# Performance work log

Measured on AMD Instinct MI355X. Metric: run time of the kernel, lower is better.

The kernel has to match this reference:

```python
import jax, jax.numpy as jnp
import numpy as np

N_NODES = 100000
N_EDGES = 1200000
D = 64
EPS = 1e-7
BETA = 1.0


def setup_inputs() -> dict:
    key = jax.random.key(0)
    k1, k2, k3, k4, k5 = jax.random.split(key, 5)
    node_feats = jax.random.normal(k1, (N_NODES, D), dtype=jnp.float32)
    edge_feats = jax.random.normal(k2, (N_EDGES, D), dtype=jnp.float32)
    W = jax.random.normal(k3, (D, D), dtype=jnp.float32) * (1.0 / np.sqrt(D))
    b = jnp.zeros((D,), dtype=jnp.float32)
    scale = jnp.ones((1,), dtype=jnp.float32)
    src = jax.random.randint(k4, (N_EDGES,), 0, N_NODES, dtype=jnp.int32)
    dst = jnp.sort(jax.random.randint(k5, (N_EDGES,), 0, N_NODES, dtype=jnp.int32))
    return {"node_feats": node_feats, "edge_feats": edge_feats, "W": W, "b": b,
            "scale": scale, "src": src, "dst": dst}


def reference(node_feats, edge_feats, W, b, scale, src, dst):
    # u_add_e: message = h[src] + edge_feats, then relu + eps  -> [E, D]
    m = jax.nn.relu(node_feats[src] + edge_feats) + EPS
    z = m * BETA
    # edge_softmax: per-destination, per-channel softmax over incoming edges
    mx = jax.ops.segment_max(z, dst, num_segments=N_NODES)      # [N, D]
    mx = jnp.where(jnp.isfinite(mx), mx, 0.0)                   # zero-degree guard
    e = jnp.exp(z - mx[dst])
    denom = jax.ops.segment_sum(e, dst, num_segments=N_NODES)   # [N, D]
    a = e / denom[dst]
    # weighted scatter-sum aggregation
    agg = jax.ops.segment_sum(m * a, dst, num_segments=N_NODES)  # [N, D]
    # MessageNorm: l2-normalize msg, rescale by ||node_feats||_2 * scale
    msg = agg / jnp.maximum(jnp.linalg.norm(agg, axis=-1, keepdims=True), 1e-12)
    feats_norm = jnp.linalg.norm(node_feats, axis=-1, keepdims=True)
    msg = msg * feats_norm * scale
    feats = node_feats + msg
    # mlp_layers=1 -> single Linear
    return feats @ W.T + b
```

## Files before the change

kernel.cpp:

```cpp
#include <hip/hip_runtime.h>

#define NN 100000
#define NE 1200000
#define DD 64
#define EPSV 1e-7f
#define NGROUPS (NN / 4)
#define GRID_BLOCKS 2048

typedef float nfloat4 __attribute__((ext_vector_type(4)));

__global__ __launch_bounds__(256)
void build_offsets(const int* __restrict__ dst, int* __restrict__ off) {
    int i = blockIdx.x * 256 + threadIdx.x;
    if (i >= NE) return;
    int d = dst[i];
    int prev = (i == 0) ? -1 : dst[i - 1];
    for (int n = prev + 1; n <= d; ++n) off[n] = i;
    if (i == NE - 1) {
        for (int n = d + 1; n <= NN; ++n) off[n] = NE;
    }
}

template<int NB>
__device__ __forceinline__ void edge_round(int base, int ee, int eg, int cg,
                                           const int* __restrict__ src,
                                           const nfloat4* __restrict__ ef4,
                                           const float4* __restrict__ nf4,
                                           float* sp, float* wp)
{
    int     sk[NB];
    nfloat4 efv[NB];
    bool    okv[NB];
    #pragma unroll
    for (int u = 0; u < NB; ++u) {
        int i = base + u * 4 + eg;
        bool ok = i < ee;
        okv[u] = ok;
        int ic = ok ? i : base;
        sk[u]  = src[ic];
        efv[u] = __builtin_nontemporal_load(&ef4[(size_t)ic * 16 + cg]);
    }
    float4 nfv[NB];
    #pragma unroll
    for (int u = 0; u < NB; ++u)
        nfv[u] = nf4[(size_t)sk[u] * 16 + cg];
    #pragma unroll
    for (int u = 0; u < NB; ++u) {
        const float* np = (const float*)&nfv[u];
        #pragma unroll
        for (int t = 0; t < 4; ++t) {
            float v = fmaxf(np[t] + efv[u][t], 0.f) + EPSV;
            float e = okv[u] ? __expf(v) : 0.f;
            sp[t] += e;
            wp[t] += e * v;
        }
    }
}

__global__ __launch_bounds__(256, 4)
void genconv_kernel(const float* __restrict__ node_feats,
                    const float* __restrict__ edge_feats,
                    const float* __restrict__ W,
                    const float* __restrict__ b,
                    const float* __restrict__ scale,
                    const int* __restrict__ src,
                    const int* __restrict__ dst,
                    const int* __restrict__ off,
                    float* __restrict__ out)
{
    __shared__ float Wt[64 * 65];
    __shared__ float featL[4 * 64];
    const int tid = threadIdx.x;

    #pragma unroll
    for (int r = 0; r < 16; ++r) {
        int idx = r * 256 + tid;
        Wt[(idx & 63) * 65 + (idx >> 6)] = W[idx];
    }

    const int wave = tid >> 6;
    const int lane = tid & 63;
    const int eg = lane >> 4;
    const int cg = lane & 15;
    const float4*  nf4 = (const float4*)node_feats;
    const nfloat4* ef4 = (const nfloat4*)edge_feats;
    const float bl = b[lane];
    const float sc = scale[0];

    __syncthreads();

    int g = blockIdx.x;
    if (g >= NGROUPS) return;

    int n = g * 4 + wave;
    int es, ee;
    if (off) { es = off[n]; ee = off[n + 1]; }
    else {
        int target = (lane < 32) ? n : (n + 1);
        int lo = 0, hi = NE;
        while (lo < hi) { int mid = (lo + hi) >> 1;
                          if (dst[mid] < target) lo = mid + 1; else hi = mid; }
        es = __shfl(lo, 0, 64); ee = __shfl(lo, 32, 64);
    }
    float4 h4 = nf4[(size_t)n * 16 + cg];

    while (true) {
        const int gn = g + gridDim.x;
        const bool have_next = gn < NGROUPS;
        int es_n = 0, ee_n = 0;
        float4 h4_n = {0.f, 0.f, 0.f, 0.f};
        if (have_next) {
            int n2 = gn * 4 + wave;
            if (off) { es_n = off[n2]; ee_n = off[n2 + 1]; }
            else {
                int target = (lane < 32) ? n2 : (n2 + 1);
                int lo = 0, hi = NE;
                while (lo < hi) { int mid = (lo + hi) >> 1;
                                  if (dst[mid] < target) lo = mid + 1; else hi = mid; }
                es_n = __shfl(lo, 0, 64); ee_n = __shfl(lo, 32, 64);
            }
            h4_n = nf4[(size_t)n2 * 16 + cg];
        }

        float4 ssum = {0.f, 0.f, 0.f, 0.f};
        float4 wsum = {0.f, 0.f, 0.f, 0.f};
        float* sp = (float*)&ssum;
        float* wp = (float*)&wsum;
        const int deg = ee - es;

        if (deg > 0) {
            if (deg <= 8) {
                edge_round<2>(es, ee, eg, cg, src, ef4, nf4, sp, wp);
            } else {
                edge_round<4>(es, ee, eg, cg, src, ef4, nf4, sp, wp);
                for (int base = es + 16; base < ee; base += 8)
                    edge_round<2>(base, ee, eg, cg, src, ef4, nf4, sp, wp);
            }
        }

        float4 agg;
        float* ap = (float*)&agg;
        #pragma unroll
        for (int t = 0; t < 4; ++t) {
            sp[t] += __shfl_xor(sp[t], 16, 64);
            sp[t] += __shfl_xor(sp[t], 32, 64);
            wp[t] += __shfl_xor(wp[t], 16, 64);
            wp[t] += __shfl_xor(wp[t], 32, 64);
            ap[t] = (sp[t] > 0.f) ? (wp[t] / sp[t]) : 0.f;
        }

        float* hp = (float*)&h4;
        float a2 = ap[0]*ap[0] + ap[1]*ap[1] + ap[2]*ap[2] + ap[3]*ap[3];
        float h2 = hp[0]*hp[0] + hp[1]*hp[1] + hp[2]*hp[2] + hp[3]*hp[3];
        #pragma unroll
        for (int o = 8; o >= 1; o >>= 1) {
            a2 += __shfl_xor(a2, o, 64);
            h2 += __shfl_xor(h2, o, 64);
        }
        float k = sqrtf(h2) * sc / fmaxf(sqrtf(a2), 1e-12f);

        float4 feat;
        float* fp = (float*)&feat;
        #pragma unroll
        for (int t = 0; t < 4; ++t) fp[t] = hp[t] + ap[t] * k;

        if (eg == 0) *(float4*)&featL[wave * 64 + cg * 4] = feat;

        float acc = bl;
        #pragma unroll
        for (int c4 = 0; c4 < 16; ++c4) {
            float4 f = *(const float4*)&featL[wave * 64 + c4 * 4];
            const float* fq = (const float*)&f;
            #pragma unroll
            for (int t = 0; t < 4; ++t)
                acc = fmaf(fq[t], Wt[(c4 * 4 + t) * 65 + lane], acc);
        }
        __builtin_nontemporal_store(acc, &out[(size_t)n * DD + lane]);

        if (!have_next) break;
        g = gn; n = gn * 4 + wave; es = es_n; ee = ee_n; h4 = h4_n;
    }
}

extern "C" void kernel_launch(void* const* d_in, const int* in_sizes, int n_in,
                              void* d_out, int out_size, void* d_ws, size_t ws_size,
                              hipStream_t stream) {
    const float* node_feats = (const float*)d_in[0];
    const float* edge_feats = (const float*)d_in[1];
    const float* W          = (const float*)d_in[2];
    const float* b          = (const float*)d_in[3];
    const float* scale      = (const float*)d_in[4];
    const int*   src        = (const int*)d_in[5];
    const int*   dst        = (const int*)d_in[6];
    float*       out        = (float*)d_out;

    int* off = nullptr;
    if (ws_size >= (size_t)(NN + 1) * sizeof(int)) {
        off = (int*)d_ws;
        build_offsets<<<(NE + 255) / 256, 256, 0, stream>>>(dst, off);
    }
    const int blocks = (GRID_BLOCKS < NGROUPS) ? GRID_BLOCKS : NGROUPS;
    genconv_kernel<<<blocks, 256, 0, stream>>>(node_feats, edge_feats, W, b,
                                               scale, src, dst, off, out);
}
```

Baseline: 462.5 us.

## Replace persistent grid-stride loop with one block per four-node group

Measured after the change: 459.2 us. No clear change (-0.7%).

```diff
diff --git a/kernel.cpp b/kernel.cpp
--- a/kernel.cpp
+++ b/kernel.cpp
@@ -4,8 +4,6 @@
 #define NE 1200000
 #define DD 64
 #define EPSV 1e-7f
-#define NGROUPS (NN / 4)
-#define GRID_BLOCKS 2048
 
 typedef float nfloat4 __attribute__((ext_vector_type(4)));
 
@@ -57,7 +55,7 @@
     }
 }
 
-__global__ __launch_bounds__(256, 4)
+__global__ __launch_bounds__(256, 6)
 void genconv_kernel(const float* __restrict__ node_feats,
                     const float* __restrict__ edge_feats,
                     const float* __restrict__ W,
@@ -80,47 +78,33 @@
 
     const int wave = tid >> 6;
     const int lane = tid & 63;
+    const int n = blockIdx.x * 4 + wave;
+    const bool active = (n < NN);
+
     const int eg = lane >> 4;
     const int cg = lane & 15;
     const float4*  nf4 = (const float4*)node_feats;
     const nfloat4* ef4 = (const nfloat4*)edge_feats;
-    const float bl = b[lane];
-    const float sc = scale[0];
 
-    __syncthreads();
+    float acc = b[lane];
 
-    int g = blockIdx.x;
-    if (g >= NGROUPS) return;
+    if (active) {
+        int es, ee;
+        if (off) {
+            es = off[n];
+            ee = off[n + 1];
+        } else {
+            int target = (lane < 32) ? n : (n + 1);
+            int lo = 0, hi = NE;
+            while (lo < hi) {
+                int mid = (lo + hi) >> 1;
+                if (dst[mid] < target) lo = mid + 1; else hi = mid;
+            }
+            es = __shfl(lo, 0, 64);
+            ee = __shfl(lo, 32, 64);
+        }
 
-    int n = g * 4 + wave;
-    int es, ee;
-    if (off) { es = off[n]; ee = off[n + 1]; }
-    else {
-        int target = (lane < 32) ? n : (n + 1);
-        int lo = 0, hi = NE;
-        while (lo < hi) { int mid = (lo + hi) >> 1;
-                          if (dst[mid] < target) lo = mid + 1; else hi = mid; }
-        es = __shfl(lo, 0, 64); ee = __shfl(lo, 32, 64);
-    }
-    float4 h4 = nf4[(size_t)n * 16 + cg];
-
-    while (true) {
-        const int gn = g + gridDim.x;
-        const bool have_next = gn < NGROUPS;
-        int es_n = 0, ee_n = 0;
-        float4 h4_n = {0.f, 0.f, 0.f, 0.f};
-        if (have_next) {
-            int n2 = gn * 4 + wave;
-            if (off) { es_n = off[n2]; ee_n = off[n2 + 1]; }
-            else {
-                int target = (lane < 32) ? n2 : (n2 + 1);
-                int lo = 0, hi = NE;
-                while (lo < hi) { int mid = (lo + hi) >> 1;
-                                  if (dst[mid] < target) lo = mid + 1; else hi = mid; }
-                es_n = __shfl(lo, 0, 64); ee_n = __shfl(lo, 32, 64);
-            }
-            h4_n = nf4[(size_t)n2 * 16 + cg];
-        }
+        float4 h4 = nf4[(size_t)n * 16 + cg];
 
         float4 ssum = {0.f, 0.f, 0.f, 0.f};
         float4 wsum = {0.f, 0.f, 0.f, 0.f};
@@ -157,7 +141,7 @@
             a2 += __shfl_xor(a2, o, 64);
             h2 += __shfl_xor(h2, o, 64);
         }
-        float k = sqrtf(h2) * sc / fmaxf(sqrtf(a2), 1e-12f);
+        float k = sqrtf(h2) * scale[0] / fmaxf(sqrtf(a2), 1e-12f);
 
         float4 feat;
         float* fp = (float*)&feat;
@@ -165,8 +149,11 @@
         for (int t = 0; t < 4; ++t) fp[t] = hp[t] + ap[t] * k;
 
         if (eg == 0) *(float4*)&featL[wave * 64 + cg * 4] = feat;
+    }
 
-        float acc = bl;
+    __syncthreads();
+
+    if (active) {
         #pragma unroll
         for (int c4 = 0; c4 < 16; ++c4) {
             float4 f = *(const float4*)&featL[wave * 64 + c4 * 4];
@@ -176,9 +163,6 @@
                 acc = fmaf(fq[t], Wt[(c4 * 4 + t) * 65 + lane], acc);
         }
         __builtin_nontemporal_store(acc, &out[(size_t)n * DD + lane]);
-
-        if (!have_next) break;
-        g = gn; n = gn * 4 + wave; es = es_n; ee = ee_n; h4 = h4_n;
     }
 }
 
@@ -199,7 +183,7 @@
         off = (int*)d_ws;
         build_offsets<<<(NE + 255) / 256, 256, 0, stream>>>(dst, off);
     }
-    const int blocks = (GRID_BLOCKS < NGROUPS) ? GRID_BLOCKS : NGROUPS;
+    const int blocks = (NN + 3) / 4;
     genconv_kernel<<<blocks, 256, 0, stream>>>(node_feats, edge_feats, W, b,
                                                scale, src, dst, off, out);
 }
```
